# Kernel tuning notes

Measured on AMD Instinct MI355X. Metric: run time of the kernel, lower is better.

The kernel has to match this reference:

```python
import jax, jax.numpy as jnp
import numpy as np

B, S, D, UNITS = 64, 2048, 1024, 1024


def setup_inputs() -> dict:
    key = jax.random.key(0)
    ks = jax.random.split(key, 5)
    sc = 1.0 / np.sqrt(D)
    return {
        "s_prev": jax.random.normal(ks[0], (B, D), jnp.float32),
        "hidden_states": jax.random.normal(ks[1], (B, S, D), jnp.float32),
        "W_kernel": jax.random.normal(ks[2], (D, UNITS), jnp.float32) * sc,
        "W_bias": jnp.zeros((UNITS,), jnp.float32),
        "U_kernel": jax.random.normal(ks[3], (D, UNITS), jnp.float32) * sc,
        "U_bias": jnp.zeros((UNITS,), jnp.float32),
        "V_kernel": jax.random.normal(ks[4], (UNITS, 1), jnp.float32) * (1.0 / np.sqrt(UNITS)),
        "V_bias": jnp.zeros((1,), jnp.float32),
    }


def reference(s_prev, hidden_states, W_kernel, W_bias, U_kernel, U_bias, V_kernel, V_bias):
    # W(s_prev): [B, units], broadcast over seq axis
    w_s = (s_prev @ W_kernel + W_bias)[:, None, :]          # [B, 1, units]
    u_h = jnp.einsum('bsd,du->bsu', hidden_states, U_kernel) + U_bias  # [B, S, units]
    scores = jnp.tanh(w_s + u_h) @ V_kernel + V_bias        # [B, S, 1]
    weight = jax.nn.softmax(scores, axis=1)                 # [B, S, 1]
    context = jnp.sum(hidden_states * weight, axis=1)       # [B, D]
    return (context, weight)
```

## Files before the change

### kernel.cpp

```cpp
#include <hip/hip_runtime.h>
#include <stdint.h>

#define NB 64
#define NS 2048
#define ND 1024
#define NU 1024

typedef __attribute__((ext_vector_type(8))) _Float16 f16x8;
typedef __attribute__((ext_vector_type(4))) _Float16 f16x4;
typedef __attribute__((ext_vector_type(4))) float f32x4;

__device__ __forceinline__ void gload_lds16(const void* g, void* l) {
    __builtin_amdgcn_global_load_lds(
        (const __attribute__((address_space(1))) unsigned int*)g,
        (__attribute__((address_space(3))) unsigned int*)l, 16, 0, 0);
}

__global__ void convert_h(const float* __restrict__ h, _Float16* __restrict__ hf, size_t n8) {
    size_t i = (size_t)blockIdx.x * blockDim.x + threadIdx.x;
    size_t stride = (size_t)gridDim.x * blockDim.x;
    for (; i < n8; i += stride) {
        const float4* p = (const float4*)(h + i * 8);
        float4 a = p[0], b = p[1];
        union { _Float16 e[8]; uint4 v; } o;
        o.e[0] = (_Float16)a.x; o.e[1] = (_Float16)a.y;
        o.e[2] = (_Float16)a.z; o.e[3] = (_Float16)a.w;
        o.e[4] = (_Float16)b.x; o.e[5] = (_Float16)b.y;
        o.e[6] = (_Float16)b.z; o.e[7] = (_Float16)b.w;
        *(uint4*)(hf + i * 8) = o.v;
    }
}

__global__ void transpose_u(const float* __restrict__ Uk, _Float16* __restrict__ Ut) {
    __shared__ float tile[64][65];
    int d0 = blockIdx.x * 64, u0 = blockIdx.y * 64;
    int tid = threadIdx.x;
    #pragma unroll
    for (int i = 0; i < 16; ++i) {
        int idx = i * 256 + tid;
        int r = idx >> 6, c = idx & 63;
        tile[r][c] = Uk[(size_t)(d0 + r) * NU + (u0 + c)];
    }
    __syncthreads();
    #pragma unroll
    for (int i = 0; i < 16; ++i) {
        int idx = i * 256 + tid;
        int c = idx >> 6, r = idx & 63;
        Ut[(size_t)(u0 + c) * ND + (d0 + r)] = (_Float16)tile[r][c];
    }
}

__global__ void prep_off(const float* __restrict__ s_prev, const float* __restrict__ Wk,
                         const float* __restrict__ Wb, const float* __restrict__ Ub,
                         float* __restrict__ off) {
    int blk = blockIdx.x;
    int b = blk >> 2, ut = blk & 3;
    int tid = threadIdx.x;
    int u = ut * 256 + tid;
    __shared__ float sp[ND];
    #pragma unroll
    for (int i = tid; i < ND; i += 256) sp[i] = s_prev[(size_t)b * ND + i];
    __syncthreads();
    float acc = 0.f;
    #pragma unroll 8
    for (int d = 0; d < ND; ++d) acc += sp[d] * Wk[(size_t)d * NU + u];
    off[(size_t)b * NU + u] = acc + Wb[u] + Ub[u];
}

__launch_bounds__(512, 2)
__global__ void scores_big(const _Float16* __restrict__ hf,
                           const _Float16* __restrict__ Ut,
                           const float* __restrict__ off,
                           const float* __restrict__ V,
                           float* __restrict__ scores)
{
    int hw = blockIdx.x;
    int chunk = gridDim.x >> 3;
    int logical = (hw & 7) * chunk + (hw >> 3);
    int ublk = logical & 3;
    int t2 = logical >> 2;
    int sblk = t2 & 7;
    int b = t2 >> 3;
    int s0 = sblk * 256, u0 = ublk * 256;

    __shared__ _Float16 As[3][256][32];
    __shared__ _Float16 Bs[3][256][32];

    int tid = threadIdx.x;
    int w = tid >> 6, l = tid & 63;
    int wr = w >> 2, wc = w & 3;
    int rg = l >> 4, cl = l & 15;

    f32x4 acc[8][4] = {};

    const _Float16* srcA[2];
    const _Float16* srcB[2];
    #pragma unroll
    for (int i = 0; i < 2; ++i) {
        int row = w * 32 + i * 16 + (l >> 2);
        int gs = ((l & 3) ^ ((row >> 1) & 3)) * 8;
        srcA[i] = hf + ((size_t)b * NS + s0 + row) * ND + gs;
        srcB[i] = Ut + (size_t)(u0 + row) * ND + gs;
    }

    #define STAGE(BUF, KK) { \
        _Pragma("unroll") \
        for (int i = 0; i < 2; ++i) { \
            gload_lds16((const void*)(srcA[i] + (KK) * 32), (void*)&As[BUF][w * 32 + i * 16][0]); \
            gload_lds16((const void*)(srcB[i] + (KK) * 32), (void*)&Bs[BUF][w * 32 + i * 16][0]); \
        } \
    }

    #define COMPUTE(BUF) { \
        f16x8 af[8], bf[4]; \
        _Pragma("unroll") \
        for (int m = 0; m < 8; ++m) { \
            int r_ = wr * 128 + m * 16 + cl; \
            af[m] = *(const f16x8*)&As[BUF][r_][(rg ^ ((r_ >> 1) & 3)) * 8]; \
        } \
        _Pragma("unroll") \
        for (int n = 0; n < 4; ++n) { \
            int r_ = wc * 64 + n * 16 + cl; \
            bf[n] = *(const f16x8*)&Bs[BUF][r_][(rg ^ ((r_ >> 1) & 3)) * 8]; \
        } \
        __builtin_amdgcn_s_setprio(1); \
        _Pragma("unroll") \
        for (int m = 0; m < 8; ++m) \
            _Pragma("unroll") \
            for (int n = 0; n < 4; ++n) \
                acc[m][n] = __builtin_amdgcn_mfma_f32_16x16x32_f16(af[m], bf[n], acc[m][n], 0, 0, 0); \
        __builtin_amdgcn_s_setprio(0); \
    }

    STAGE(0, 0);
    STAGE(1, 1);

    int bi = 0;
    for (int t = 0; t < 30; ++t) {
        asm volatile("s_waitcnt vmcnt(4)" ::: "memory");
        __builtin_amdgcn_sched_barrier(0);
        __builtin_amdgcn_s_barrier();
        __builtin_amdgcn_sched_barrier(0);
        int bn = bi + 2; if (bn >= 3) bn -= 3;
        STAGE(bn, t + 2);
        __builtin_amdgcn_sched_barrier(0);
        COMPUTE(bi);
        ++bi; if (bi == 3) bi = 0;
    }
    asm volatile("s_waitcnt vmcnt(4)" ::: "memory");
    __builtin_amdgcn_sched_barrier(0);
    __builtin_amdgcn_s_barrier();
    __builtin_amdgcn_sched_barrier(0);
    COMPUTE(bi);
    ++bi; if (bi == 3) bi = 0;
    asm volatile("s_waitcnt vmcnt(0)" ::: "memory");
    __builtin_amdgcn_sched_barrier(0);
    __builtin_amdgcn_s_barrier();
    __builtin_amdgcn_sched_barrier(0);
    COMPUTE(bi);

    #undef STAGE
    #undef COMPUTE

    float offv[4], vv[4];
    #pragma unroll
    for (int n = 0; n < 4; ++n) {
        int u = u0 + wc * 64 + n * 16 + cl;
        offv[n] = off[(size_t)b * NU + u];
        vv[n] = V[u];
    }
    #pragma unroll
    for (int m = 0; m < 8; ++m) {
        #pragma unroll
        for (int i = 0; i < 4; ++i) {
            float sacc = 0.f;
            #pragma unroll
            for (int n = 0; n < 4; ++n) {
                float x = acc[m][n][i] + offv[n];
                float t = 1.0f - 2.0f / (1.0f + __expf(2.0f * x));
                sacc += t * vv[n];
            }
            #pragma unroll
            for (int msk = 1; msk < 16; msk <<= 1) sacc += __shfl_xor(sacc, msk, 64);
            if (cl == 0)
                atomicAdd(&scores[(size_t)b * NS + s0 + wr * 128 + m * 16 + rg * 4 + i], sacc);
        }
    }
}

__launch_bounds__(256, 4)
__global__ void scores_kernel(const float* __restrict__ h,
                              const _Float16* __restrict__ Ut,
                              const float* __restrict__ off,
                              const float* __restrict__ V,
                              float* __restrict__ scores)
{
    int hw = blockIdx.x;
    int chunk = gridDim.x >> 3;
    int logical = (hw & 7) * chunk + (hw >> 3);
    int ublk = logical & 7;
    int t2 = logical >> 3;
    int sblk = t2 & 15;
    int b = t2 >> 4;
    int s0 = sblk * 128, u0 = ublk * 128;

    __shared__ _Float16 As[2][128][32];
    __shared__ _Float16 Bs[3][128][32];

    int tid = threadIdx.x;
    int w = tid >> 6, l = tid & 63;
    int wr = w >> 1, wc = w & 1;
    int rg = l >> 4, cl = l & 15;

    f32x4 acc[4][4] = {};

    const float* hA = h + ((size_t)b * NS + s0) * ND;
    int arow = tid >> 3;
    int acol4 = (tid & 7) * 4;
    int aslog = (tid & 7) >> 1;
    int ahalf = tid & 1;
    const _Float16* srcB[2];
    #pragma unroll
    for (int i = 0; i < 2; ++i) {
        int row = w * 32 + i * 16 + (l >> 2);
        srcB[i] = Ut + (size_t)(u0 + row) * ND + (((l & 3) ^ ((row >> 1) & 3)) * 8);
    }

    float4 av[4];

    #define LOADA(KK) { \
        _Pragma("unroll") \
        for (int p = 0; p < 4; ++p) \
            av[p] = *(const float4*)(hA + (size_t)(p * 32 + arow) * ND + (KK) * 32 + acol4); \
    }
    #define ISSUEB(BI, KK) { \
        _Pragma("unroll") \
        for (int i = 0; i < 2; ++i) \
            gload_lds16((const void*)(srcB[i] + (KK) * 32), (void*)&Bs[BI][w * 32 + i * 16][0]); \
    }
    #define CVTW(ABUF) { \
        _Pragma("unroll") \
        for (int p = 0; p < 4; ++p) { \
            int r_ = p * 32 + arow; \
            int sp_ = aslog ^ ((r_ >> 1) & 3); \
            union { _Float16 e[4]; uint2 u2; } cv; \
            cv.e[0] = (_Float16)av[p].x; cv.e[1] = (_Float16)av[p].y; \
            cv.e[2] = (_Float16)av[p].z; cv.e[3] = (_Float16)av[p].w; \
            *(uint2*)&As[ABUF][r_][sp_ * 8 + ahalf * 4] = cv.u2; \
        } \
    }
    #define COMPUTE(ABUF, BI) { \
        f16x8 af[4], bf[4]; \
        _Pragma("unroll") \
        for (int m = 0; m < 4; ++m) { \
            int r_ = wr * 64 + m * 16 + cl; \
            af[m] = *(const f16x8*)&As[ABUF][r_][(rg ^ ((r_ >> 1) & 3)) * 8]; \
        } \
        _Pragma("unroll") \
        for (int n = 0; n < 4; ++n) { \
            int r_ = wc * 64 + n * 16 + cl; \
            bf[n] = *(const f16x8*)&Bs[BI][r_][(rg ^ ((r_ >> 1) & 3)) * 8]; \
        } \
        _Pragma("unroll") \
        for (int m = 0; m < 4; ++m) \
            _Pragma("unroll") \
            for (int n = 0; n < 4; ++n) \
                acc[m][n] = __builtin_amdgcn_mfma_f32_16x16x32_f16(af[m], bf[n], acc[m][n], 0, 0, 0); \
    }

    LOADA(0);
    ISSUEB(0, 0);
    int bcur = 0;
    for (int t = 0; t < 31; ++t) {
        asm volatile("s_waitcnt vmcnt(2)" ::: "memory");
        __builtin_amdgcn_sched_barrier(0);
        CVTW(t & 1);
        LOADA(t + 1);
        int bnxt = bcur + 1; if (bnxt == 3) bnxt = 0;
        ISSUEB(bnxt, t + 1);
        asm volatile("s_waitcnt vmcnt(6) lgkmcnt(0)" ::: "memory");
        __builtin_amdgcn_sched_barrier(0);
        __builtin_amdgcn_s_barrier();
        __builtin_amdgcn_sched_barrier(0);
        COMPUTE(t & 1, bcur);
        bcur = bnxt;
    }
    asm volatile("s_waitcnt vmcnt(0)" ::: "memory");
    __builtin_amdgcn_sched_barrier(0);
    CVTW(1);
    asm volatile("s_waitcnt lgkmcnt(0)" ::: "memory");
    __builtin_amdgcn_sched_barrier(0);
    __builtin_amdgcn_s_barrier();
    __builtin_amdgcn_sched_barrier(0);
    COMPUTE(1, bcur);

    #undef LOADA
    #undef ISSUEB
    #undef CVTW
    #undef COMPUTE

    float offv[4], vv[4];
    #pragma unroll
    for (int n = 0; n < 4; ++n) {
        int u = u0 + wc * 64 + n * 16 + cl;
        offv[n] = off[(size_t)b * NU + u];
        vv[n] = V[u];
    }
    #pragma unroll
    for (int m = 0; m < 4; ++m) {
        #pragma unroll
        for (int i = 0; i < 4; ++i) {
            float sacc = 0.f;
            #pragma unroll
            for (int n = 0; n < 4; ++n) {
                float x = acc[m][n][i] + offv[n];
                float t = 1.0f - 2.0f / (1.0f + __expf(2.0f * x));
                sacc += t * vv[n];
            }
            #pragma unroll
            for (int msk = 1; msk < 16; msk <<= 1) sacc += __shfl_xor(sacc, msk, 64);
            if (cl == 0)
                atomicAdd(&scores[(size_t)b * NS + s0 + wr * 64 + m * 16 + rg * 4 + i], sacc);
        }
    }
}

__global__ void softmax_kernel(const float* __restrict__ scores, float* __restrict__ outw) {
    int b = blockIdx.x, tid = threadIdx.x;
    const float* src = scores + (size_t)b * NS;
    float4 x0 = *(const float4*)(src + tid * 8);
    float4 x1 = *(const float4*)(src + tid * 8 + 4);
    float m = fmaxf(fmaxf(fmaxf(x0.x, x0.y), fmaxf(x0.z, x0.w)),
                    fmaxf(fmaxf(x1.x, x1.y), fmaxf(x1.z, x1.w)));
    #pragma unroll
    for (int msk = 1; msk < 64; msk <<= 1) m = fmaxf(m, __shfl_xor(m, msk, 64));
    __shared__ float redm[4], reds[4];
    if ((tid & 63) == 0) redm[tid >> 6] = m;
    __syncthreads();
    m = fmaxf(fmaxf(redm[0], redm[1]), fmaxf(redm[2], redm[3]));
    float e[8];
    e[0] = __expf(x0.x - m); e[1] = __expf(x0.y - m); e[2] = __expf(x0.z - m); e[3] = __expf(x0.w - m);
    e[4] = __expf(x1.x - m); e[5] = __expf(x1.y - m); e[6] = __expf(x1.z - m); e[7] = __expf(x1.w - m);
    float s = e[0] + e[1] + e[2] + e[3] + e[4] + e[5] + e[6] + e[7];
    #pragma unroll
    for (int msk = 1; msk < 64; msk <<= 1) s += __shfl_xor(s, msk, 64);
    if ((tid & 63) == 0) reds[tid >> 6] = s;
    __syncthreads();
    float Z = reds[0] + reds[1] + reds[2] + reds[3];
    float r = 1.0f / Z;
    float4 o0 = { e[0] * r, e[1] * r, e[2] * r, e[3] * r };
    float4 o1 = { e[4] * r, e[5] * r, e[6] * r, e[7] * r };
    *(float4*)(outw + (size_t)b * NS + tid * 8) = o0;
    *(float4*)(outw + (size_t)b * NS + tid * 8 + 4) = o1;
}

__global__ void context_partial_f16(const _Float16* __restrict__ hf, const float* __restrict__ wgt,
                                    float* __restrict__ part) {
    int sc = blockIdx.x, b = blockIdx.y, tid = threadIdx.x;
    __shared__ float lw[128];
    if (tid < 128) lw[tid] = wgt[(size_t)b * NS + sc * 128 + tid];
    __syncthreads();
    const _Float16* hb = hf + ((size_t)b * NS + sc * 128) * ND + tid * 4;
    float4 acc = { 0.f, 0.f, 0.f, 0.f };
    #pragma unroll 4
    for (int s = 0; s < 128; ++s) {
        f16x4 hv = *(const f16x4*)(hb + (size_t)s * ND);
        float wv = lw[s];
        acc.x += (float)hv[0] * wv; acc.y += (float)hv[1] * wv;
        acc.z += (float)hv[2] * wv; acc.w += (float)hv[3] * wv;
    }
    *(float4*)(part + ((size_t)(sc * NB + b)) * ND + tid * 4) = acc;
}

__global__ void context_partial(const float* __restrict__ h, const float* __restrict__ wgt,
                                float* __restrict__ part) {
    int sc = blockIdx.x, b = blockIdx.y, tid = threadIdx.x;
    __shared__ float lw[128];
    if (tid < 128) lw[tid] = wgt[(size_t)b * NS + sc * 128 + tid];
    __syncthreads();
    const float* hb = h + ((size_t)b * NS + sc * 128) * ND + tid * 4;
    float4 acc = { 0.f, 0.f, 0.f, 0.f };
    #pragma unroll 4
    for (int s = 0; s < 128; ++s) {
        float4 hv = *(const float4*)(hb + (size_t)s * ND);
        float wv = lw[s];
        acc.x += hv.x * wv; acc.y += hv.y * wv; acc.z += hv.z * wv; acc.w += hv.w * wv;
    }
    *(float4*)(part + ((size_t)(sc * NB + b)) * ND + tid * 4) = acc;
}

__global__ void context_reduce(const float* __restrict__ part, float* __restrict__ outc) {
    int b = blockIdx.x, tid = threadIdx.x;
    float4 acc = { 0.f, 0.f, 0.f, 0.f };
    #pragma unroll
    for (int k = 0; k < 16; ++k) {
        float4 p = *(const float4*)(part + ((size_t)(k * NB + b)) * ND + tid * 4);
        acc.x += p.x; acc.y += p.y; acc.z += p.z; acc.w += p.w;
    }
    *(float4*)(outc + (size_t)b * ND + tid * 4) = acc;
}

extern "C" void kernel_launch(void* const* d_in, const int* in_sizes, int n_in,
                              void* d_out, int out_size, void* d_ws, size_t ws_size,
                              hipStream_t stream) {
    const float* s_prev = (const float*)d_in[0];
    const float* hidden = (const float*)d_in[1];
    const float* Wk     = (const float*)d_in[2];
    const float* Wb     = (const float*)d_in[3];
    const float* Uk     = (const float*)d_in[4];
    const float* Ub     = (const float*)d_in[5];
    const float* Vk     = (const float*)d_in[6];

    float* out_ctx = (float*)d_out;
    float* out_w   = out_ctx + NB * ND;

    char* ws = (char*)d_ws;
    _Float16* Ut  = (_Float16*)ws;
    float* off    = (float*)(ws + (size_t)(2 << 20));
    float* scores = (float*)(ws + (size_t)(2 << 20) + (256 << 10));
    float* part   = (float*)(ws + (size_t)(2 << 20) + (768 << 10));
    size_t small  = (size_t)(2 << 20) + (768 << 10) + (4 << 20);
    _Float16* hf16 = (_Float16*)(ws + small);
    size_t hbytes = (size_t)NB * NS * ND * sizeof(_Float16);

    bool fast = (ws_size >= small + hbytes);

    hipMemsetAsync(scores, 0, (size_t)NB * NS * sizeof(float), stream);
    transpose_u<<<dim3(16, 16), 256, 0, stream>>>(Uk, Ut);
    prep_off<<<256, 256, 0, stream>>>(s_prev, Wk, Wb, Ub, off);

    if (fast) {
        size_t n8 = (size_t)NB * NS * ND / 8;
        convert_h<<<8192, 256, 0, stream>>>(hidden, hf16, n8);
        scores_big<<<2048, 512, 0, stream>>>(hf16, Ut, off, Vk, scores);
        softmax_kernel<<<NB, 256, 0, stream>>>(scores, out_w);
        context_partial_f16<<<dim3(16, NB), 256, 0, stream>>>(hf16, out_w, part);
    } else {
        scores_kernel<<<8192, 256, 0, stream>>>(hidden, Ut, off, Vk, scores);
        softmax_kernel<<<NB, 256, 0, stream>>>(scores, out_w);
        context_partial<<<dim3(16, NB), 256, 0, stream>>>(hidden, out_w, part);
    }
    context_reduce<<<NB, 256, 0, stream>>>(part, out_ctx);
}
```

Before: 684.2 us.

## Restructure scores GEMM main loop into finer-grained interleaved load/compute phases

Replaces the three-buffer, one-barrier-per-k-step pipeline in the scores GEMM with a double-buffered scheme over 64-wide k tiles, each split into two 32-wide sub-steps and two M-halves. Global-to-LDS loads for A and B are issued between MFMA groups, with explicit waitcnt and barriers at each phase. The aim is to hide LDS reads and global loads behind MFMA work more finely, similar to an eight-phase ping-pong schedule. In exchange it adds more barriers per iteration, and the final iteration reissues redundant loads of tile 15.

```diff
diff --git a/kernel.cpp b/kernel.cpp
--- a/kernel.cpp
+++ b/kernel.cpp
@@ -68,7 +68,7 @@
 }
 
 __launch_bounds__(512, 2)
-__global__ void scores_big(const _Float16* __restrict__ hf,
+__global__ void scores_8ph(const _Float16* __restrict__ hf,
                            const _Float16* __restrict__ Ut,
                            const float* __restrict__ off,
                            const float* __restrict__ V,
@@ -83,8 +83,8 @@
     int b = t2 >> 3;
     int s0 = sblk * 256, u0 = ublk * 256;
 
-    __shared__ _Float16 As[3][256][32];
-    __shared__ _Float16 Bs[3][256][32];
+    __shared__ _Float16 As[2][2][2][128][32];
+    __shared__ _Float16 Bs[2][2][2][128][32];
 
     int tid = threadIdx.x;
     int w = tid >> 6, l = tid & 63;
@@ -93,74 +93,79 @@
 
     f32x4 acc[8][4] = {};
 
-    const _Float16* srcA[2];
-    const _Float16* srcB[2];
-    #pragma unroll
-    for (int i = 0; i < 2; ++i) {
-        int row = w * 32 + i * 16 + (l >> 2);
-        int gs = ((l & 3) ^ ((row >> 1) & 3)) * 8;
-        srcA[i] = hf + ((size_t)b * NS + s0 + row) * ND + gs;
-        srcB[i] = Ut + (size_t)(u0 + row) * ND + gs;
-    }
-
-    #define STAGE(BUF, KK) { \
-        _Pragma("unroll") \
-        for (int i = 0; i < 2; ++i) { \
-            gload_lds16((const void*)(srcA[i] + (KK) * 32), (void*)&As[BUF][w * 32 + i * 16][0]); \
-            gload_lds16((const void*)(srcB[i] + (KK) * 32), (void*)&Bs[BUF][w * 32 + i * 16][0]); \
-        } \
-    }
-
-    #define COMPUTE(BUF) { \
-        f16x8 af[8], bf[4]; \
-        _Pragma("unroll") \
-        for (int m = 0; m < 8; ++m) { \
-            int r_ = wr * 128 + m * 16 + cl; \
-            af[m] = *(const f16x8*)&As[BUF][r_][(rg ^ ((r_ >> 1) & 3)) * 8]; \
-        } \
+    int srow = tid >> 2;
+    int gslot = (tid & 3) ^ ((srow >> 1) & 3);
+    const _Float16* srcA0 = hf + ((size_t)b * NS + s0 + srow) * ND + gslot * 8;
+    const _Float16* srcB0 = Ut + (size_t)(u0 + srow) * ND + gslot * 8;
+
+    #define STAGE_A(DB, KS, TT) { \
+        gload_lds16((const void*)(srcA0 + (TT) * 64 + (KS) * 32), \
+                    (void*)((_Float16*)As[DB][KS][0] + tid * 8)); \
+        gload_lds16((const void*)(srcA0 + (size_t)128 * ND + (TT) * 64 + (KS) * 32), \
+                    (void*)((_Float16*)As[DB][KS][1] + tid * 8)); }
+    #define STAGE_B(DB, KS, TT) { \
+        gload_lds16((const void*)(srcB0 + (TT) * 64 + (KS) * 32), \
+                    (void*)((_Float16*)Bs[DB][KS][0] + tid * 8)); \
+        gload_lds16((const void*)(srcB0 + (size_t)128 * ND + (TT) * 64 + (KS) * 32), \
+                    (void*)((_Float16*)Bs[DB][KS][1] + tid * 8)); }
+
+    #define READ_B(DB, KS, bfv) { \
         _Pragma("unroll") \
         for (int n = 0; n < 4; ++n) { \
-            int r_ = wc * 64 + n * 16 + cl; \
-            bf[n] = *(const f16x8*)&Bs[BUF][r_][(rg ^ ((r_ >> 1) & 3)) * 8]; \
-        } \
+            int rb = (wc & 1) * 64 + n * 16 + cl; \
+            bfv[n] = *(const f16x8*)&Bs[DB][KS][wc >> 1][rb][(rg ^ ((rb >> 1) & 3)) * 8]; \
+        } }
+    #define READ_A(DB, KS, MH, afv) { \
+        _Pragma("unroll") \
+        for (int mm = 0; mm < 4; ++mm) { \
+            int ra = (MH) * 64 + mm * 16 + cl; \
+            afv[mm] = *(const f16x8*)&As[DB][KS][wr][ra][(rg ^ ((ra >> 1) & 3)) * 8]; \
+        } }
+    #define MFMA_Q(MH, afv, bfv) { \
         __builtin_amdgcn_s_setprio(1); \
         _Pragma("unroll") \
-        for (int m = 0; m < 8; ++m) \
+        for (int mm = 0; mm < 4; ++mm) \
             _Pragma("unroll") \
             for (int n = 0; n < 4; ++n) \
-                acc[m][n] = __builtin_amdgcn_mfma_f32_16x16x32_f16(af[m], bf[n], acc[m][n], 0, 0, 0); \
-        __builtin_amdgcn_s_setprio(0); \
-    }
-
-    STAGE(0, 0);
-    STAGE(1, 1);
-
-    int bi = 0;
-    for (int t = 0; t < 30; ++t) {
-        asm volatile("s_waitcnt vmcnt(4)" ::: "memory");
-        __builtin_amdgcn_sched_barrier(0);
-        __builtin_amdgcn_s_barrier();
-        __builtin_amdgcn_sched_barrier(0);
-        int bn = bi + 2; if (bn >= 3) bn -= 3;
-        STAGE(bn, t + 2);
-        __builtin_amdgcn_sched_barrier(0);
-        COMPUTE(bi);
-        ++bi; if (bi == 3) bi = 0;
-    }
-    asm volatile("s_waitcnt vmcnt(4)" ::: "memory");
-    __builtin_amdgcn_sched_barrier(0);
-    __builtin_amdgcn_s_barrier();
-    __builtin_amdgcn_sched_barrier(0);
-    COMPUTE(bi);
-    ++bi; if (bi == 3) bi = 0;
+                acc[(MH) * 4 + mm][n] = \
+                    __builtin_amdgcn_mfma_f32_16x16x32_f16(afv[mm], bfv[n], acc[(MH) * 4 + mm][n], 0, 0, 0); \
+        __builtin_amdgcn_s_setprio(0); }
+
+    STAGE_A(0, 0, 0); STAGE_B(0, 0, 0); STAGE_A(0, 1, 0); STAGE_B(0, 1, 0);
+
+    for (int T = 0; T < 16; ++T) {
+        int d = T & 1, dn = d ^ 1;
+        int TN = (T < 15) ? T + 1 : 15;
+        #pragma unroll
+        for (int ks = 0; ks < 2; ++ks) {
+            f16x8 bf[4], af0[4], af1[4];
+            STAGE_A(dn, ks, TN);
+            asm volatile("s_waitcnt vmcnt(6)" ::: "memory");
+            __builtin_amdgcn_sched_barrier(0);
+            __builtin_amdgcn_s_barrier();
+            __builtin_amdgcn_sched_barrier(0);
+            READ_B(d, ks, bf);
+            READ_A(d, ks, 0, af0);
+            asm volatile("s_waitcnt lgkmcnt(0)" ::: "memory");
+            __builtin_amdgcn_sched_barrier(0);
+            MFMA_Q(0, af0, bf);
+            STAGE_B(dn, ks, TN);
+            READ_A(d, ks, 1, af1);
+            __builtin_amdgcn_s_barrier();
+            asm volatile("s_waitcnt lgkmcnt(0)" ::: "memory");
+            __builtin_amdgcn_sched_barrier(0);
+            MFMA_Q(1, af1, bf);
+            __builtin_amdgcn_s_barrier();
+        }
+    }
     asm volatile("s_waitcnt vmcnt(0)" ::: "memory");
     __builtin_amdgcn_sched_barrier(0);
-    __builtin_amdgcn_s_barrier();
-    __builtin_amdgcn_sched_barrier(0);
-    COMPUTE(bi);
-
-    #undef STAGE
-    #undef COMPUTE
+
+    #undef STAGE_A
+    #undef STAGE_B
+    #undef READ_B
+    #undef READ_A
+    #undef MFMA_Q
 
     float offv[4], vv[4];
     #pragma unroll
@@ -432,7 +437,7 @@
     if (fast) {
         size_t n8 = (size_t)NB * NS * ND / 8;
         convert_h<<<8192, 256, 0, stream>>>(hidden, hf16, n8);
-        scores_big<<<2048, 512, 0, stream>>>(hf16, Ut, off, Vk, scores);
+        scores_8ph<<<2048, 512, 0, stream>>>(hf16, Ut, off, Vk, scores);
         softmax_kernel<<<NB, 256, 0, stream>>>(scores, out_w);
         context_partial_f16<<<dim3(16, NB), 256, 0, stream>>>(hf16, out_w, part);
     } else {
```

Measured after the change: 645.8 us. 1.06x faster.
